# Kernel tuning notes

Measured on AMD Instinct MI355X. Metric: run time of the kernel, lower is better.

## Reference

```python
import jax, jax.numpy as jnp
import numpy as np

NUM_HEADS = 12
HEAD_DIM = 64  # d_out // num_heads = 768 // 12


def setup_inputs() -> dict:
    key = jax.random.key(0)
    ks = jax.random.split(key, 6)
    b, s, d = 2, 2048, 768
    x = jax.random.normal(ks[0], (b, s, d), dtype=jnp.float32)
    sc = 1.0 / np.sqrt(d)
    Wq = jax.random.normal(ks[1], (d, d), dtype=jnp.float32) * sc
    Wk = jax.random.normal(ks[2], (d, d), dtype=jnp.float32) * sc
    Wv = jax.random.normal(ks[3], (d, d), dtype=jnp.float32) * sc
    Wo = jax.random.normal(ks[4], (d, d), dtype=jnp.float32) * sc
    bo = jnp.zeros((d,), dtype=jnp.float32)
    return {"x": x, "Wq": Wq, "Wk": Wk, "Wv": Wv, "Wo": Wo, "bo": bo}


def reference(x, Wq, Wk, Wv, Wo, bo):
    # Prefill from a fresh sliding-window KV cache: cache == new K/V,
    # standard causal (triu) mask. dropout=0 (eval).
    b, s, d = x.shape
    H, Dh = NUM_HEADS, HEAD_DIM

    def proj(W):  # torch Linear: x @ W^T, then split heads -> [b, H, s, Dh]
        return (x @ W.T).reshape(b, s, H, Dh).transpose(0, 2, 1, 3)

    q, k, v = proj(Wq), proj(Wk), proj(Wv)

    scores = jnp.einsum('bhqd,bhkd->bhqk', q, k)          # [b,H,s,s]
    causal = jnp.triu(jnp.ones((s, s), dtype=bool), k=1)  # future positions
    scores = jnp.where(causal[None, None], -jnp.inf, scores)
    attn = jax.nn.softmax(scores / np.sqrt(Dh), axis=-1)

    ctx = jnp.einsum('bhqk,bhkd->bhqd', attn, v)          # [b,H,s,Dh]
    ctx = ctx.transpose(0, 2, 1, 3).reshape(b, s, d)      # [b,s,d_out]
    return ctx @ Wo.T + bo
```

## Files before the change

kernel.cpp:

```cpp
#include <hip/hip_runtime.h>
#include <stdint.h>

typedef __attribute__((ext_vector_type(4))) float f32x4;
typedef __attribute__((ext_vector_type(8))) short s16x8;

#if __has_builtin(__builtin_amdgcn_exp2f)
#define EXP2(x) __builtin_amdgcn_exp2f(x)
#else
#define EXP2(x) exp2f(x)
#endif

#define GL2LDS(g, s)                                                        \
  __builtin_amdgcn_global_load_lds(                                         \
      (const __attribute__((address_space(1))) void*)(g),                   \
      (__attribute__((address_space(3))) void*)(s), 16, 0, 0)

__device__ __forceinline__ unsigned short tobf(float x) {
  uint32_t u = __builtin_bit_cast(uint32_t, x);
  u += 0x7fffu + ((u >> 16) & 1u);
  return (unsigned short)(u >> 16);
}

__device__ __forceinline__ uint32_t pk2(float lo, float hi) {
  return (uint32_t)tobf(lo) | ((uint32_t)tobf(hi) << 16);
}

__device__ __forceinline__ uint32_t pktrunc(float lo, float hi) {
  return __builtin_amdgcn_perm(__builtin_bit_cast(uint32_t, hi),
                               __builtin_bit_cast(uint32_t, lo), 0x07060302u);
}

__global__ __launch_bounds__(256) void cvt_all(
    const float* __restrict__ x,  const float* __restrict__ wq,
    const float* __restrict__ wk, const float* __restrict__ wv,
    const float* __restrict__ wo, unsigned short* __restrict__ outb) {
  int i = blockIdx.x * 256 + threadIdx.x;
  if (i >= 1376256) return;
  const float* in;
  int j;
  if (i < 786432) { in = x; j = i; }
  else {
    int k = i - 786432;
    int sel = k / 147456;
    j = k - sel * 147456;
    in = (sel == 0) ? wq : (sel == 1) ? wk : (sel == 2) ? wv : wo;
  }
  float4 v = reinterpret_cast<const float4*>(in)[j];
  uint2 o; o.x = pk2(v.x, v.y); o.y = pk2(v.z, v.w);
  reinterpret_cast<uint2*>(outb)[i] = o;
}

__global__ __launch_bounds__(256) void qkv_gemm(
    const unsigned short* __restrict__ xb,
    const unsigned short* __restrict__ wq,
    const unsigned short* __restrict__ wk,
    const unsigned short* __restrict__ wv,
    unsigned short* __restrict__ q_ws,
    unsigned short* __restrict__ k_ws,
    unsigned short* __restrict__ vt_ws) {
  __shared__ unsigned short As[2][4096];
  __shared__ unsigned short Bs[2][4096];
  const int t = threadIdx.x;
  const int l = t & 63, w = t >> 6;
  const int wm = w >> 1, wn = w & 1;
  const int lr = l & 15, lg = l >> 4;

  const int id = (int)blockIdx.x;
  const int xcd = id & 7;
  const int g = id >> 3;
  const int nt = g % 18;
  const int tileM = ((g / 18) * 8 + xcd) * 128;
  const int wsel = nt / 6;
  const unsigned short* W = (wsel == 0) ? wq : ((wsel == 1) ? wk : wv);
  const int tileN = (nt % 6) * 128;

  const int srow = l >> 2;
  const int scol = ((l & 3) ^ (srow & 3)) * 8;

#define QSTAGE(buf, k0_)                                                       \
  do {                                                                         \
    _Pragma("unroll")                                                          \
    for (int i_ = 0; i_ < 2; ++i_) {                                           \
      GL2LDS(&xb[(tileM + w * 32 + i_ * 16 + srow) * 768 + (k0_) + scol],      \
             &As[buf][w * 1024 + i_ * 512]);                                   \
      GL2LDS(&W [(tileN + w * 32 + i_ * 16 + srow) * 768 + (k0_) + scol],      \
             &Bs[buf][w * 1024 + i_ * 512]);                                   \
    }                                                                          \
  } while (0)

  const int chf = ((lg ^ (lr & 3)) << 3);

  f32x4 acc[4][4];
  const f32x4 z4 = {0.f, 0.f, 0.f, 0.f};
#pragma unroll
  for (int i = 0; i < 4; ++i)
#pragma unroll
    for (int j = 0; j < 4; ++j) acc[i][j] = z4;

  QSTAGE(0, 0);
  __syncthreads();
  int c = 0;
  for (int it = 0; it < 24; ++it) {
    if (it < 23) QSTAGE(c ^ 1, (it + 1) * 32);
    s16x8 a[4], b[4];
#pragma unroll
    for (int mi = 0; mi < 4; ++mi)
      a[mi] = *(const s16x8*)&As[c][(wm * 64 + mi * 16 + lr) * 32 + chf];
#pragma unroll
    for (int ni = 0; ni < 4; ++ni)
      b[ni] = *(const s16x8*)&Bs[c][(wn * 64 + ni * 16 + lr) * 32 + chf];
    __builtin_amdgcn_s_setprio(1);
#pragma unroll
    for (int mi = 0; mi < 4; ++mi)
#pragma unroll
      for (int ni = 0; ni < 4; ++ni)
        acc[mi][ni] = __builtin_amdgcn_mfma_f32_16x16x32_bf16(a[mi], b[ni], acc[mi][ni], 0, 0, 0);
    __builtin_amdgcn_s_setprio(0);
    if (it < 23) {
      __syncthreads();
      c ^= 1;
    }
  }
#undef QSTAGE

#pragma unroll
  for (int mi = 0; mi < 4; ++mi)
#pragma unroll
    for (int ni = 0; ni < 4; ++ni) {
      int m0 = tileM + wm * 64 + mi * 16 + lg * 4;
      int n = tileN + wn * 64 + ni * 16 + lr;
      int bb = m0 >> 11, sq0 = m0 & 2047;
      int h = n >> 6, dh = n & 63;
      if (wsel == 0) {
#pragma unroll
        for (int r = 0; r < 4; ++r)
          q_ws[((bb * 12 + h) * 2048 + sq0 + r) * 64 + dh] =
              tobf(acc[mi][ni][r] * 0.18033688011112042f);
      } else if (wsel == 1) {
#pragma unroll
        for (int r = 0; r < 4; ++r)
          k_ws[((bb * 12 + h) * 2048 + sq0 + r) * 64 + dh] = tobf(acc[mi][ni][r]);
      } else {
        uint2 o;
        o.x = pk2(acc[mi][ni][0], acc[mi][ni][1]);
        o.y = pk2(acc[mi][ni][2], acc[mi][ni][3]);
        *(uint2*)&vt_ws[((bb * 12 + h) * 64 + dh) * 2048 + sq0] = o;
      }
    }
}

__global__ __launch_bounds__(128) void attn_kernel(
    const unsigned short* __restrict__ q_ws,
    const unsigned short* __restrict__ k_ws,
    const unsigned short* __restrict__ vt_ws,
    unsigned short* __restrict__ ctx) {
  __shared__ unsigned short Ks[2][4096];
  __shared__ unsigned short Vs[2][4096];

  const int t = threadIdx.x;
  const int l = t & 63, w = t >> 6;
  const int lr = l & 15, lg = l >> 4;

  const int id = (int)blockIdx.x;
  const int xcd = id & 7;
  const int g = id >> 3;
  const int qt = 63 - g / 3;
  const int bh = (g % 3) * 8 + xcd;

  const int rb = w * 8 + (l >> 3);
  const int gcol = ((l & 7) ^ (l >> 3)) * 8;
  const int krow = 8 * ((rb >> 2) & 3) + (rb & 3);
  const unsigned short* kgp  = &k_ws[(bh * 2048 + krow) * 64 + gcol];
  const unsigned short* vbase = &vt_ws[(bh * 64 + rb) * 2048 + gcol];

#define STAGE(buf, kt_)                                                \
  do {                                                                 \
    GL2LDS(kgp + (kt_) * 4096,           &Ks[buf][w * 512]);           \
    GL2LDS(kgp + (kt_) * 4096 + 2048,    &Ks[buf][1024 + w * 512]);    \
    GL2LDS(kgp + (kt_) * 4096 + 256,     &Ks[buf][2048 + w * 512]);    \
    GL2LDS(kgp + (kt_) * 4096 + 2304,    &Ks[buf][3072 + w * 512]);    \
    GL2LDS(vbase + (kt_) * 64,           &Vs[buf][w * 512]);           \
    GL2LDS(vbase + (kt_) * 64 + 32768,   &Vs[buf][1024 + w * 512]);    \
    GL2LDS(vbase + (kt_) * 64 + 65536,   &Vs[buf][2048 + w * 512]);    \
    GL2LDS(vbase + (kt_) * 64 + 98304,   &Vs[buf][3072 + w * 512]);    \
  } while (0)

  const int cks0 = (lg * 8) ^ ((lr & 7) << 3);
  const int cks1 = (32 + lg * 8) ^ ((lr & 7) << 3);

  const int bb = bh / 12, hh = bh % 12;
  const f32x4 z4 = {0.f, 0.f, 0.f, 0.f};

  const int ktmax = qt >> 1;
  const int qg = qt * 32 + w * 16 + lr;

  s16x8 qa[2];
#pragma unroll
  for (int kk = 0; kk < 2; ++kk)
    qa[kk] = *(const s16x8*)&q_ws[(bh * 2048 + qg) * 64 + kk * 32 + lg * 8];

  f32x4 o[4];
#pragma unroll
  for (int di = 0; di < 4; ++di) o[di] = z4;
  float lrun = 0.f;
  f32x4 s[4];

  STAGE(0, 0);
  __syncthreads();

  __builtin_amdgcn_s_setprio(1);
#pragma unroll
  for (int ni = 0; ni < 4; ++ni) {
    s16x8 kb0 = *(const s16x8*)&Ks[0][ni * 1024 + lr * 64 + cks0];
    s16x8 kb1 = *(const s16x8*)&Ks[0][ni * 1024 + lr * 64 + cks1];
    s[ni] = __builtin_amdgcn_mfma_f32_16x16x32_bf16(kb0, qa[0], z4, 0, 0, 0);
    s[ni] = __builtin_amdgcn_mfma_f32_16x16x32_bf16(kb1, qa[1], s[ni], 0, 0, 0);
  }
  __builtin_amdgcn_s_setprio(0);
  if (ktmax >= 1) STAGE(1, 1);

  int c = 0;
  for (int kt = 0; kt <= ktmax; ++kt) {
    if (kt == ktmax) {
#pragma unroll
      for (int ni = 0; ni < 4; ++ni)
#pragma unroll
        for (int r = 0; r < 4; ++r) {
          int kg_ = kt * 64 + ((ni & 1) << 5) + (lg << 3) + ((ni >> 1) << 2) + r;
          if (kg_ > qg) s[ni][r] = -1e30f;
        }
    }

#pragma unroll
    for (int ni = 0; ni < 4; ++ni)
#pragma unroll
      for (int r = 0; r < 4; ++r) s[ni][r] = EXP2(s[ni][r]);
    {
      float t0 = (s[0][0] + s[0][1]) + (s[0][2] + s[0][3]);
      float t1 = (s[1][0] + s[1][1]) + (s[1][2] + s[1][3]);
      float t2 = (s[2][0] + s[2][1]) + (s[2][2] + s[2][3]);
      float t3 = (s[3][0] + s[3][1]) + (s[3][2] + s[3][3]);
      lrun += (t0 + t1) + (t2 + t3);
    }

    s16x8 pa[2];
#pragma unroll
    for (int kk = 0; kk < 2; ++kk) {
      uint4 u;
      u.x = pktrunc(s[kk][0],     s[kk][1]);
      u.y = pktrunc(s[kk][2],     s[kk][3]);
      u.z = pktrunc(s[kk + 2][0], s[kk + 2][1]);
      u.w = pktrunc(s[kk + 2][2], s[kk + 2][3]);
      pa[kk] = __builtin_bit_cast(s16x8, u);
    }

    const bool have_next = (kt < ktmax);
    __builtin_amdgcn_s_setprio(1);
    if (have_next) {
      __syncthreads();
#pragma unroll
      for (int ni = 0; ni < 4; ++ni) {
        s16x8 kb0 = *(const s16x8*)&Ks[c ^ 1][ni * 1024 + lr * 64 + cks0];
        s16x8 kb1 = *(const s16x8*)&Ks[c ^ 1][ni * 1024 + lr * 64 + cks1];
        s[ni] = __builtin_amdgcn_mfma_f32_16x16x32_bf16(kb0, qa[0], z4, 0, 0, 0);
        s[ni] = __builtin_amdgcn_mfma_f32_16x16x32_bf16(kb1, qa[1], s[ni], 0, 0, 0);
      }
    }
#pragma unroll
    for (int di = 0; di < 4; ++di) {
      s16x8 vb0 = *(const s16x8*)&Vs[c][di * 1024 + lr * 64 + cks0];
      s16x8 vb1 = *(const s16x8*)&Vs[c][di * 1024 + lr * 64 + cks1];
      o[di] = __builtin_amdgcn_mfma_f32_16x16x32_bf16(vb0, pa[0], o[di], 0, 0, 0);
      o[di] = __builtin_amdgcn_mfma_f32_16x16x32_bf16(vb1, pa[1], o[di], 0, 0, 0);
    }
    __builtin_amdgcn_s_setprio(0);

    if (kt + 2 <= ktmax) {
      __syncthreads();
      STAGE(c, kt + 2);
    }
    c ^= 1;
  }

  float lt = lrun + __shfl_xor(lrun, 16);
  lt += __shfl_xor(lt, 32);
  const float rl = 1.0f / lt;
#pragma unroll
  for (int di = 0; di < 4; ++di) {
    uint2 ov;
    ov.x = pk2(o[di][0] * rl, o[di][1] * rl);
    ov.y = pk2(o[di][2] * rl, o[di][3] * rl);
    *(uint2*)&ctx[(bb * 2048 + qg) * 768 + hh * 64 + di * 16 + lg * 4] = ov;
  }
#undef STAGE
}

__global__ __launch_bounds__(256) void out_gemm(
    const unsigned short* __restrict__ ctxb,
    const unsigned short* __restrict__ wo,
    const float* __restrict__ bo,
    float* __restrict__ out) {
  __shared__ unsigned short As[2][4096];
  __shared__ unsigned short Bs[2][4096];
  const int t = threadIdx.x;
  const int l = t & 63, w = t >> 6;
  const int wm = w >> 1, wn = w & 1;
  const int lr = l & 15, lg = l >> 4;

  const int id = (int)blockIdx.x;
  const int xcd = id & 7;
  const int g = id >> 3;
  const int tileM = ((g / 6) * 8 + xcd) * 128;
  const int tileN = (g % 6) * 128;

  const int srow = l >> 2;
  const int scol = ((l & 3) ^ (srow & 3)) * 8;

#define OSTAGE(buf, k0_)                                                       \
  do {                                                                         \
    _Pragma("unroll")                                                          \
    for (int i_ = 0; i_ < 2; ++i_) {                                           \
      GL2LDS(&ctxb[(tileM + w * 32 + i_ * 16 + srow) * 768 + (k0_) + scol],    \
             &As[buf][w * 1024 + i_ * 512]);                                   \
      GL2LDS(&wo  [(tileN + w * 32 + i_ * 16 + srow) * 768 + (k0_) + scol],    \
             &Bs[buf][w * 1024 + i_ * 512]);                                   \
    }                                                                          \
  } while (0)

  const int chf = ((lg ^ (lr & 3)) << 3);

  f32x4 acc[4][4];
  const f32x4 z4 = {0.f, 0.f, 0.f, 0.f};
#pragma unroll
  for (int i = 0; i < 4; ++i)
#pragma unroll
    for (int j = 0; j < 4; ++j) acc[i][j] = z4;

  OSTAGE(0, 0);
  __syncthreads();
  int c = 0;
  for (int it = 0; it < 24; ++it) {
    if (it < 23) OSTAGE(c ^ 1, (it + 1) * 32);
    s16x8 a[4], b[4];
#pragma unroll
    for (int mi = 0; mi < 4; ++mi)
      a[mi] = *(const s16x8*)&As[c][(wm * 64 + mi * 16 + lr) * 32 + chf];
#pragma unroll
    for (int ni = 0; ni < 4; ++ni)
      b[ni] = *(const s16x8*)&Bs[c][(wn * 64 + ni * 16 + lr) * 32 + chf];
    __builtin_amdgcn_s_setprio(1);
#pragma unroll
    for (int mi = 0; mi < 4; ++mi)
#pragma unroll
      for (int ni = 0; ni < 4; ++ni)
        acc[mi][ni] = __builtin_amdgcn_mfma_f32_16x16x32_bf16(a[mi], b[ni], acc[mi][ni], 0, 0, 0);
    __builtin_amdgcn_s_setprio(0);
    if (it < 23) {
      __syncthreads();
      c ^= 1;
    }
  }
#undef OSTAGE

#pragma unroll
  for (int mi = 0; mi < 4; ++mi)
#pragma unroll
    for (int ni = 0; ni < 4; ++ni)
#pragma unroll
      for (int r = 0; r < 4; ++r) {
        int m = tileM + wm * 64 + mi * 16 + lg * 4 + r;
        int n = tileN + wn * 64 + ni * 16 + lr;
        out[m * 768 + n] = acc[mi][ni][r] + bo[n];
      }
}

extern "C" void kernel_launch(void* const* d_in, const int* in_sizes, int n_in,
                              void* d_out, int out_size, void* d_ws, size_t ws_size,
                              hipStream_t stream) {
  const float* x  = (const float*)d_in[0];
  const float* Wq = (const float*)d_in[1];
  const float* Wk = (const float*)d_in[2];
  const float* Wv = (const float*)d_in[3];
  const float* Wo = (const float*)d_in[4];
  const float* bo = (const float*)d_in[5];
  float* out = (float*)d_out;

  char* ws = (char*)d_ws;
  unsigned short* xb    = (unsigned short*)(ws);
  unsigned short* wqb   = (unsigned short*)(ws + 6291456);
  unsigned short* wkb   = (unsigned short*)(ws + 7471104);
  unsigned short* wvb   = (unsigned short*)(ws + 8650752);
  unsigned short* wob   = (unsigned short*)(ws + 9830400);
  unsigned short* q_ws  = (unsigned short*)(ws + 11010048);
  unsigned short* k_ws  = (unsigned short*)(ws + 17301504);
  unsigned short* vt_ws = (unsigned short*)(ws + 23592960);
  unsigned short* ctx   = (unsigned short*)(ws + 29884416);

  cvt_all<<<5376, 256, 0, stream>>>(x, Wq, Wk, Wv, Wo, (unsigned short*)ws);
  qkv_gemm<<<576, 256, 0, stream>>>(xb, wqb, wkb, wvb, q_ws, k_ws, vt_ws);
  attn_kernel<<<1536, 128, 0, stream>>>(q_ws, k_ws, vt_ws, ctx);
  out_gemm<<<192, 256, 0, stream>>>(ctx, wob, bo, out);
}
```

Before: 86.12 us.

## Shrink GEMM tiles to raise block count for QKV and output projections

The QKV GEMM moves from 128x128 tiles with 4 waves to 64x128 tiles with 2 waves, doubling the grid to 1152 blocks. The output GEMM moves from 128x128 tiles with 4 waves to 64x64 tiles with a single wave, growing the grid from 192 to 768 blocks. The aim is to fill the machine's many CUs better, since the output GEMM previously launched fewer blocks than there are CUs. The cost is less operand reuse per tile, more global and LDS traffic per FLOP, and little latency hiding inside each block.

```diff
diff --git a/kernel.cpp b/kernel.cpp
--- a/kernel.cpp
+++ b/kernel.cpp
@@ -50,7 +50,7 @@
   reinterpret_cast<uint2*>(outb)[i] = o;
 }
 
-__global__ __launch_bounds__(256) void qkv_gemm(
+__global__ __launch_bounds__(128) void qkv_gemm(
     const unsigned short* __restrict__ xb,
     const unsigned short* __restrict__ wq,
     const unsigned short* __restrict__ wk,
@@ -58,34 +58,32 @@
     unsigned short* __restrict__ q_ws,
     unsigned short* __restrict__ k_ws,
     unsigned short* __restrict__ vt_ws) {
-  __shared__ unsigned short As[2][4096];
+  __shared__ unsigned short As[2][2048];
   __shared__ unsigned short Bs[2][4096];
   const int t = threadIdx.x;
   const int l = t & 63, w = t >> 6;
-  const int wm = w >> 1, wn = w & 1;
   const int lr = l & 15, lg = l >> 4;
 
   const int id = (int)blockIdx.x;
   const int xcd = id & 7;
   const int g = id >> 3;
   const int nt = g % 18;
-  const int tileM = ((g / 18) * 8 + xcd) * 128;
+  const int tileM = ((g / 18) * 8 + xcd) * 64;
   const int wsel = nt / 6;
   const unsigned short* W = (wsel == 0) ? wq : ((wsel == 1) ? wk : wv);
   const int tileN = (nt % 6) * 128;
 
-  const int srow = l >> 2;
-  const int scol = ((l & 3) ^ (srow & 3)) * 8;
+  const int srow = w * 16 + (l >> 2);
+  const int scol = ((l & 3) ^ ((l >> 2) & 3)) * 8;
 
 #define QSTAGE(buf, k0_)                                                       \
   do {                                                                         \
+    GL2LDS(&xb[(tileM + srow) * 768 + (k0_) + scol],       &As[buf][w * 512]); \
+    GL2LDS(&xb[(tileM + 32 + srow) * 768 + (k0_) + scol],  &As[buf][1024 + w * 512]); \
     _Pragma("unroll")                                                          \
-    for (int i_ = 0; i_ < 2; ++i_) {                                           \
-      GL2LDS(&xb[(tileM + w * 32 + i_ * 16 + srow) * 768 + (k0_) + scol],      \
-             &As[buf][w * 1024 + i_ * 512]);                                   \
-      GL2LDS(&W [(tileN + w * 32 + i_ * 16 + srow) * 768 + (k0_) + scol],      \
-             &Bs[buf][w * 1024 + i_ * 512]);                                   \
-    }                                                                          \
+    for (int i_ = 0; i_ < 4; ++i_)                                             \
+      GL2LDS(&W[(tileN + i_ * 32 + srow) * 768 + (k0_) + scol],                \
+             &Bs[buf][i_ * 1024 + w * 512]);                                   \
   } while (0)
 
   const int chf = ((lg ^ (lr & 3)) << 3);
@@ -105,10 +103,10 @@
     s16x8 a[4], b[4];
 #pragma unroll
     for (int mi = 0; mi < 4; ++mi)
-      a[mi] = *(const s16x8*)&As[c][(wm * 64 + mi * 16 + lr) * 32 + chf];
+      a[mi] = *(const s16x8*)&As[c][(mi * 16 + lr) * 32 + chf];
 #pragma unroll
     for (int ni = 0; ni < 4; ++ni)
-      b[ni] = *(const s16x8*)&Bs[c][(wn * 64 + ni * 16 + lr) * 32 + chf];
+      b[ni] = *(const s16x8*)&Bs[c][(w * 64 + ni * 16 + lr) * 32 + chf];
     __builtin_amdgcn_s_setprio(1);
 #pragma unroll
     for (int mi = 0; mi < 4; ++mi)
@@ -127,8 +125,8 @@
   for (int mi = 0; mi < 4; ++mi)
 #pragma unroll
     for (int ni = 0; ni < 4; ++ni) {
-      int m0 = tileM + wm * 64 + mi * 16 + lg * 4;
-      int n = tileN + wn * 64 + ni * 16 + lr;
+      int m0 = tileM + mi * 16 + lg * 4;
+      int n = tileN + w * 64 + ni * 16 + lr;
       int bb = m0 >> 11, sq0 = m0 & 2047;
       int h = n >> 6, dh = n & 63;
       if (wsel == 0) {
@@ -295,23 +293,21 @@
 #undef STAGE
 }
 
-__global__ __launch_bounds__(256) void out_gemm(
+__global__ __launch_bounds__(64) void out_gemm(
     const unsigned short* __restrict__ ctxb,
     const unsigned short* __restrict__ wo,
     const float* __restrict__ bo,
     float* __restrict__ out) {
-  __shared__ unsigned short As[2][4096];
-  __shared__ unsigned short Bs[2][4096];
-  const int t = threadIdx.x;
-  const int l = t & 63, w = t >> 6;
-  const int wm = w >> 1, wn = w & 1;
+  __shared__ unsigned short As[2][2048];
+  __shared__ unsigned short Bs[2][2048];
+  const int l = threadIdx.x;
   const int lr = l & 15, lg = l >> 4;
 
   const int id = (int)blockIdx.x;
   const int xcd = id & 7;
   const int g = id >> 3;
-  const int tileM = ((g / 6) * 8 + xcd) * 128;
-  const int tileN = (g % 6) * 128;
+  const int tileN = (g % 12) * 64;
+  const int tileM = ((g / 12) * 8 + xcd) * 64;
 
   const int srow = l >> 2;
   const int scol = ((l & 3) ^ (srow & 3)) * 8;
@@ -319,11 +315,11 @@
 #define OSTAGE(buf, k0_)                                                       \
   do {                                                                         \
     _Pragma("unroll")                                                          \
-    for (int i_ = 0; i_ < 2; ++i_) {                                           \
-      GL2LDS(&ctxb[(tileM + w * 32 + i_ * 16 + srow) * 768 + (k0_) + scol],    \
-             &As[buf][w * 1024 + i_ * 512]);                                   \
-      GL2LDS(&wo  [(tileN + w * 32 + i_ * 16 + srow) * 768 + (k0_) + scol],    \
-             &Bs[buf][w * 1024 + i_ * 512]);                                   \
+    for (int i_ = 0; i_ < 4; ++i_) {                                           \
+      GL2LDS(&ctxb[(tileM + i_ * 16 + srow) * 768 + (k0_) + scol],             \
+             &As[buf][i_ * 512]);                                              \
+      GL2LDS(&wo  [(tileN + i_ * 16 + srow) * 768 + (k0_) + scol],             \
+             &Bs[buf][i_ * 512]);                                              \
     }                                                                          \
   } while (0)
 
@@ -344,10 +340,10 @@
     s16x8 a[4], b[4];
 #pragma unroll
     for (int mi = 0; mi < 4; ++mi)
-      a[mi] = *(const s16x8*)&As[c][(wm * 64 + mi * 16 + lr) * 32 + chf];
+      a[mi] = *(const s16x8*)&As[c][(mi * 16 + lr) * 32 + chf];
 #pragma unroll
     for (int ni = 0; ni < 4; ++ni)
-      b[ni] = *(const s16x8*)&Bs[c][(wn * 64 + ni * 16 + lr) * 32 + chf];
+      b[ni] = *(const s16x8*)&Bs[c][(ni * 16 + lr) * 32 + chf];
     __builtin_amdgcn_s_setprio(1);
 #pragma unroll
     for (int mi = 0; mi < 4; ++mi)
@@ -368,8 +364,8 @@
     for (int ni = 0; ni < 4; ++ni)
 #pragma unroll
       for (int r = 0; r < 4; ++r) {
-        int m = tileM + wm * 64 + mi * 16 + lg * 4 + r;
-        int n = tileN + wn * 64 + ni * 16 + lr;
+        int m = tileM + mi * 16 + lg * 4 + r;
+        int n = tileN + ni * 16 + lr;
         out[m * 768 + n] = acc[mi][ni][r] + bo[n];
       }
 }
@@ -397,7 +393,7 @@
   unsigned short* ctx   = (unsigned short*)(ws + 29884416);
 
   cvt_all<<<5376, 256, 0, stream>>>(x, Wq, Wk, Wv, Wo, (unsigned short*)ws);
-  qkv_gemm<<<576, 256, 0, stream>>>(xb, wqb, wkb, wvb, q_ws, k_ws, vt_ws);
+  qkv_gemm<<<1152, 128, 0, stream>>>(xb, wqb, wkb, wvb, q_ws, k_ws, vt_ws);
   attn_kernel<<<1536, 128, 0, stream>>>(q_ws, k_ws, vt_ws, ctx);
-  out_gemm<<<192, 256, 0, stream>>>(ctx, wob, bo, out);
-}
+  out_gemm<<<768, 64, 0, stream>>>(ctx, wob, bo, out);
+}
```

After: 88.96 us. +3.3%, slower.
